# Optimization experiments

Measured on AMD Instinct MI355X. Metric: run time of the kernel, lower is better.

## Reference

```python
import jax, jax.numpy as jnp
import numpy as np

K = 0.5            # init kwarg k (score threshold)
G, S, C, M, DE = 256, 128, 512, 384, 128
N = G * S          # total nodes
EG = S + M         # edges per graph (first S point at the graph's last 'super' node)
E = G * EG


def setup_inputs() -> dict:
    key = jax.random.key(0)
    ks = jax.random.split(key, 8)
    x = jax.random.normal(ks[0], (N, C), jnp.float32)
    W = jax.random.normal(ks[1], (1, C), jnp.float32)
    batch = jnp.repeat(jnp.arange(G, dtype=jnp.int32), S)
    edge_num = jnp.full((G,), EG, dtype=jnp.int32)
    off = jnp.arange(G, dtype=jnp.int32) * S
    # structured edges: node i -> last node of its graph (the 'super node')
    struct_src = off[:, None] + jnp.arange(S, dtype=jnp.int32)[None, :]
    struct_dst = jnp.broadcast_to((off + S - 1)[:, None], (G, S))
    rand_src = jax.random.randint(ks[2], (G, M), 0, S, jnp.int32) + off[:, None]
    rand_dst = jax.random.randint(ks[3], (G, M), 0, S, jnp.int32) + off[:, None]
    src = jnp.concatenate([struct_src, rand_src], axis=1).reshape(-1)
    dst = jnp.concatenate([struct_dst, rand_dst], axis=1).reshape(-1)
    edge_index = jnp.stack([src, dst], axis=0)  # [2, E], grouped per graph
    edge_inform = jax.random.normal(ks[4], (E, DE), jnp.float32)
    br_feature = jax.random.normal(ks[5], (N, C), jnp.float32)
    return dict(x=x, edge_index=edge_index, edge_num=edge_num, edge_inform=edge_inform,
                batch=batch, br_feature=br_feature, br_index=edge_index,
                br_batch=batch, br_com_num=jnp.zeros((G,), jnp.int32), W=W)


def reference(x, edge_index, edge_num, edge_inform, batch, br_feature, br_index, br_batch, br_com_num, W):
    n, e, g = x.shape[0], edge_index.shape[1], edge_num.shape[0]
    score = jax.nn.sigmoid(jnp.mean(x * W, axis=-1))          # [N]
    x_out = x * score[:, None] * 2.0

    # per-graph node layout
    counts = jnp.bincount(batch, length=g)
    node_off = jnp.cumsum(counts) - counts
    last_node = node_off + counts - 1                          # 'super node' of each graph
    is_last = jnp.zeros((n,), bool).at[last_node].set(True)
    # torch loop runs over all but the last node of each graph
    low = (score < K) & (~is_last)                             # [N]

    # per-graph edge layout
    e_graph = jnp.repeat(jnp.arange(g, dtype=edge_num.dtype), edge_num)
    e_off = jnp.cumsum(edge_num) - edge_num
    local_pos = jnp.arange(e) - e_off[e_graph]                 # position inside graph's slice
    src, dst = edge_index[0], edge_index[1]
    # torch searches positions [1, eg) backwards for edge (low_node -> last_node): the
    # LAST matching position per low-score node gets masked out.
    cand = (dst == last_node[e_graph]) & low[src] & (batch[src] == e_graph) & (local_pos >= 1)
    val = jnp.where(cand, jnp.arange(e), -1)
    rem = jax.ops.segment_max(val, src, num_segments=n)        # last candidate edge per node
    drop = rem[rem >= 0]
    edge_mask = jnp.ones((e,), bool).at[drop].set(False)

    edge_num_plus = jax.ops.segment_sum(edge_mask.astype(edge_num.dtype), e_graph, num_segments=g)
    edge_index_plus = edge_index[:, edge_mask]
    edge_inform_plus = edge_inform[edge_mask]

    # BatchReversal: remove node (local_low_idx + com_num[g] + br_node_offset[g]) per low node
    n2 = br_feature.shape[0]
    counts2 = jnp.bincount(br_batch, length=g)
    node_off2 = jnp.cumsum(counts2) - counts2
    low_nodes = jnp.arange(n)[low]
    g_of = batch[low_nodes]
    br_drop = (low_nodes - node_off[g_of]) + br_com_num[g_of] + node_off2[g_of]
    br_mask = jnp.ones((n2,), bool).at[br_drop].set(False)
    leave = jnp.arange(n2)[br_mask]

    # filter_edge: keep nodes, remap edge endpoints, drop dangling edges
    br_feature_p = br_feature[leave]
    br_batch_p = br_batch[leave]
    remap = jnp.full((n2,), -1, dtype=jnp.int32).at[leave].set(jnp.arange(leave.shape[0], dtype=jnp.int32))
    r, c = remap[br_index[0]], remap[br_index[1]]
    keep = (r >= 0) & (c >= 0)
    br_index_p = jnp.stack([r[keep], c[keep]], axis=0)

    return (x_out, edge_index_plus, edge_inform_plus, edge_num_plus,
            br_feature_p, br_index_p, br_batch_p)
```

## Files before the change

kernel.cpp:

```cpp
#include <hip/hip_runtime.h>
#include <math.h>


__global__ void __launch_bounds__(512) k_count(
    const int* __restrict__ batch, int N,
    const int* __restrict__ br_batch, int N2,
    int* __restrict__ counts, int* __restrict__ counts2,
    int* __restrict__ dropcnt, int* __restrict__ brmask, int G){
  __shared__ int h1[512], h2[512];
  int t = threadIdx.x;
  h1[t] = 0; h2[t] = 0;
  __syncthreads();
  int gid    = blockIdx.x*blockDim.x + t;
  int stride = gridDim.x*blockDim.x;
  for (int i = gid; i < N;  i += stride) atomicAdd(&h1[batch[i]], 1);
  for (int i = gid; i < N2; i += stride) atomicAdd(&h2[br_batch[i]], 1);
  for (int i = gid; i < N2; i += stride) brmask[i] = 0;
  if (gid < G) dropcnt[gid] = 0;
  __syncthreads();
  if (t < G){
    if (h1[t]) atomicAdd(&counts[t],  h1[t]);
    if (h2[t]) atomicAdd(&counts2[t], h2[t]);
  }
}

__device__ __forceinline__ int scan512_excl_val(int v, int* s){
  int t = threadIdx.x;
  s[t] = v; __syncthreads();
  for (int off = 1; off < 512; off <<= 1){
    int add = (t >= off) ? s[t - off] : 0;
    __syncthreads();
    s[t] += add;
    __syncthreads();
  }
  int r = s[t] - v;
  __syncthreads();
  return r;
}

__global__ void __launch_bounds__(512) k_scan(
    const int* __restrict__ counts, const int* __restrict__ counts2,
    const int* __restrict__ edge_num, int G,
    int* __restrict__ node_off, int* __restrict__ node_off2,
    int* __restrict__ e_off){
  __shared__ int s[512];
  int t = threadIdx.x;
  int v1 = (t < G) ? counts[t]   : 0;
  int v2 = (t < G) ? counts2[t]  : 0;
  int v3 = (t < G) ? edge_num[t] : 0;
  int o1 = scan512_excl_val(v1, s);
  int o2 = scan512_excl_val(v2, s);
  int o3 = scan512_excl_val(v3, s);
  if (t < G){ node_off[t] = o1; node_off2[t] = o2; e_off[t] = o3; }
}

__global__ void __launch_bounds__(256) k_score(
    const float* __restrict__ x, const float* __restrict__ W,
    const int* __restrict__ batch, const int* __restrict__ counts,
    const int* __restrict__ node_off,
    float* __restrict__ out_x, int* __restrict__ low, int* __restrict__ rem,
    int C, int N){
  int wave = (blockIdx.x * blockDim.x + threadIdx.x) >> 6;
  int lane = threadIdx.x & 63;
  if (wave >= N) return;
  const float4* x4 = (const float4*)(x + (size_t)wave * C);
  const float4* W4 = (const float4*)W;
  const int nv = C >> 2;
  float acc = 0.f;
  float4 a0, a1;
  const bool fast = (nv == 128);
  if (fast){
    float4 w0 = W4[lane], w1 = W4[lane + 64];
    a0 = x4[lane]; a1 = x4[lane + 64];
    acc = a0.x*w0.x + a0.y*w0.y + a0.z*w0.z + a0.w*w0.w
        + a1.x*w1.x + a1.y*w1.y + a1.z*w1.z + a1.w*w1.w;
  } else {
    for (int k = lane; k < nv; k += 64){
      float4 a = x4[k]; float4 w = W4[k];
      acc += a.x*w.x + a.y*w.y + a.z*w.z + a.w*w.w;
    }
  }
  #pragma unroll
  for (int d = 1; d < 64; d <<= 1) acc += __shfl_xor(acc, d, 64);
  float scale = 2.0f / (1.0f + expf(-acc / (float)C));
  if (lane == 0){
    int g    = batch[wave];
    int last = node_off[g] + counts[g] - 1;
    low[wave] = (acc < 0.0f) && (wave != last) ? 1 : 0;
    rem[wave] = -1;
  }
  float4* o4 = (float4*)(out_x + (size_t)wave * C);
  if (fast){
    a0.x *= scale; a0.y *= scale; a0.z *= scale; a0.w *= scale;
    a1.x *= scale; a1.y *= scale; a1.z *= scale; a1.w *= scale;
    o4[lane]      = a0;
    o4[lane + 64] = a1;
  } else {
    for (int k = lane; k < nv; k += 64){
      float4 a = x4[k];
      a.x *= scale; a.y *= scale; a.z *= scale; a.w *= scale;
      o4[k] = a;
    }
  }
}

__device__ __forceinline__ int find_graph(const int* __restrict__ e_off, int G, int e){
  int lo = 0, hi = G - 1;
  while (lo < hi){
    int mid = (lo + hi + 1) >> 1;
    if (e_off[mid] <= e) lo = mid; else hi = mid - 1;
  }
  return lo;
}

__global__ void k_pass1(const int* __restrict__ ei, const int* __restrict__ e_off,
                        const int* __restrict__ node_off, const int* __restrict__ node_off2,
                        const int* __restrict__ counts, const int* __restrict__ batch,
                        const int* __restrict__ low, const int* __restrict__ br_com_num,
                        int* __restrict__ rem, int* __restrict__ brmask,
                        int E, int N, int G){
  int e = blockIdx.x*blockDim.x + threadIdx.x;
  if (e < N && low[e]){
    int g = batch[e];
    int d = e - node_off[g] + br_com_num[g] + node_off2[g];
    brmask[d] = 1;
  }
  if (e >= E) return;
  int g  = find_graph(e_off, G, e);
  if (e - e_off[g] < 1) return;
  int dst  = ei[E + e];
  int last = node_off[g] + counts[g] - 1;
  if (dst != last) return;
  int src = ei[e];
  if (!low[src]) return;
  if (batch[src] != g) return;
  atomicMax(&rem[src], e);
}

__global__ void k_pass2(const int* __restrict__ ei, const int* __restrict__ rem,
                        const int* __restrict__ e_off, const int* __restrict__ brmask,
                        const int* __restrict__ bi,
                        int* __restrict__ dropcnt,
                        int* __restrict__ bsumsA, int* __restrict__ bsumsB,
                        int* __restrict__ bsumsC,
                        int E, int N2, int EB, int G, int nbE, int nbN2){
  __shared__ int s[256];
  int b = blockIdx.x, t = threadIdx.x;
  int v = 0;
  if (b < nbE){
    int e = b*256 + t;
    if (e < E){
      v = (rem[ei[e]] != e) ? 1 : 0;
      if (!v){ int g = find_graph(e_off, G, e); atomicAdd(&dropcnt[g], 1); }
    }
  } else if (b < nbE + nbN2){
    int j = (b - nbE)*256 + t;
    v = (j < N2) ? (brmask[j] == 0) : 0;
  } else {
    int e = (b - nbE - nbN2)*256 + t;
    if (e < EB)
      v = (brmask[bi[e]] == 0 && brmask[bi[EB + e]] == 0) ? 1 : 0;
  }
  s[t] = v; __syncthreads();
  for (int off = 128; off > 0; off >>= 1){
    if (t < off) s[t] += s[t + off];
    __syncthreads();
  }
  if (t == 0){
    if (b < nbE)             bsumsA[b] = s[0];
    else if (b < nbE + nbN2) bsumsB[b - nbE] = s[0];
    else                     bsumsC[b - nbE - nbN2] = s[0];
  }
}

__device__ void scan_bsums_dev(int* __restrict__ bsums, int nb, int* __restrict__ total){
  __shared__ int s[1024];
  int t = threadIdx.x;
  int v = (t < nb) ? bsums[t] : 0;
  s[t] = v; __syncthreads();
  for (int off = 1; off < 1024; off <<= 1){
    int add = (t >= off) ? s[t - off] : 0;
    __syncthreads();
    s[t] += add;
    __syncthreads();
  }
  if (t < nb)      bsums[t] = s[t] - v;
  if (t == nb - 1) *total   = s[t];
}

__global__ void k_scanABC(int* __restrict__ bsumsA, int nbA,
                          int* __restrict__ bsumsB, int nbB,
                          int* __restrict__ bsumsC, int nbC,
                          int* __restrict__ totals){
  if      (blockIdx.x == 0) scan_bsums_dev(bsumsA, nbA, &totals[0]);
  else if (blockIdx.x == 1) scan_bsums_dev(bsumsB, nbB, &totals[1]);
  else                      scan_bsums_dev(bsumsC, nbC, &totals[2]);
}

__device__ __forceinline__ int excl_scan256(int v, int* s){
  int t = threadIdx.x;
  s[t] = v; __syncthreads();
  for (int off = 1; off < 256; off <<= 1){
    int add = (t >= off) ? s[t - off] : 0;
    __syncthreads();
    s[t] += add;
    __syncthreads();
  }
  return s[t] - v;
}

__global__ void k_pass3(const int* __restrict__ ei, const int* __restrict__ rem,
                        const int* __restrict__ bsumsA, const int* __restrict__ bsumsB,
                        const int* __restrict__ totals,
                        const int* __restrict__ edge_num, const int* __restrict__ dropcnt,
                        const int* __restrict__ brmask,
                        int* __restrict__ edge_pos, int* __restrict__ remap,
                        float* __restrict__ out, long long base0,
                        int E, int N2, int G, int DE, int nbE){
  __shared__ int s[256];
  int b = blockIdx.x, t = threadIdx.x;
  if (b < nbE){
    int e = b*256 + t;
    int keep = 0, src = 0, dst = 0;
    if (e < E){ src = ei[e]; dst = ei[E + e]; keep = (rem[src] != e) ? 1 : 0; }
    int excl = excl_scan256(keep, s);
    long long ek = totals[0];
    if (e < E){
      if (keep){
        int p = bsumsA[b] + excl;
        edge_pos[e] = p;
        out[base0 + p]      = (float)src;
        out[base0 + ek + p] = (float)dst;
      } else edge_pos[e] = -1;
    }
    if (b == 0){
      long long off3 = base0 + 2*ek + ek*(long long)DE;
      for (int g = t; g < G; g += 256)
        out[off3 + g] = (float)(edge_num[g] - dropcnt[g]);
    }
  } else {
    int j = (b - nbE)*256 + t;
    int keep = (j < N2) ? (brmask[j] == 0) : 0;
    int excl = excl_scan256(keep, s);
    if (j < N2) remap[j] = keep ? (bsumsB[b - nbE] + excl) : -1;
  }
}

__global__ void __launch_bounds__(256) k_pass45(
    const int* __restrict__ bi, const int* __restrict__ remap,
    const int* __restrict__ bsumsC, const int* __restrict__ totals,
    const float* __restrict__ inform, const int* __restrict__ edge_pos,
    const float* __restrict__ brf, const int* __restrict__ brb,
    float* __restrict__ out, long long base0,
    int G, int DE, int C, int EB, int E, int N2,
    int nbB, int nbE8){
  int b = blockIdx.x, t = threadIdx.x;
  long long ek = totals[0];
  if (b < nbB){
    __shared__ int s[256];
    long long nk = totals[1], kc = totals[2];
    long long off4 = base0 + 2*ek + ek*(long long)DE + G;
    int e = b*256 + t;
    int r = -1, c = -1, keep = 0;
    if (e < EB){
      r = remap[bi[e]];
      c = remap[bi[EB + e]];
      keep = (r >= 0 && c >= 0) ? 1 : 0;
    }
    int excl = excl_scan256(keep, s);
    if (keep){
      long long off5 = off4 + nk*(long long)C;
      int p = bsumsC[b] + excl;
      out[off5 + p]      = (float)r;
      out[off5 + kc + p] = (float)c;
    }
  } else if (b < nbB + nbE8){
    int e = (b - nbB)*8 + (t >> 5);
    if (e >= E) return;
    int p = edge_pos[e];
    if (p < 0) return;
    long long off2 = base0 + 2*ek;
    int lane = t & 31;
    const float4* in4 = (const float4*)(inform + (size_t)e * DE);
    float4*       o4  = (float4*)(out + off2 + (long long)p * DE);
    for (int j = lane; j < (DE >> 2); j += 32) o4[j] = in4[j];
  } else {
    long long nk = totals[1], kc = totals[2];
    long long off4 = base0 + 2*ek + ek*(long long)DE + G;
    int j = (b - nbB - nbE8)*2 + (t >> 7);
    if (j >= N2) return;
    int p = remap[j];
    if (p < 0) return;
    int lane = t & 127;
    const float4* in4 = (const float4*)(brf + (size_t)j * C);
    float4*       o4  = (float4*)(out + off4 + (long long)p * C);
    for (int k = lane; k < (C >> 2); k += 128) o4[k] = in4[k];
    if (lane == 0){
      long long off6 = off4 + nk*(long long)C + 2*kc;
      out[off6 + p] = (float)brb[j];
    }
  }
}

extern "C" void kernel_launch(void* const* d_in, const int* in_sizes, int n_in,
                              void* d_out, int out_size, void* d_ws, size_t ws_size,
                              hipStream_t stream){
  const float* x           = (const float*)d_in[0];
  const int*   edge_index  = (const int*)  d_in[1];
  const int*   edge_num    = (const int*)  d_in[2];
  const float* edge_inform = (const float*)d_in[3];
  const int*   batch       = (const int*)  d_in[4];
  const float* br_feature  = (const float*)d_in[5];
  const int*   br_index    = (const int*)  d_in[6];
  const int*   br_batch    = (const int*)  d_in[7];
  const int*   br_com_num  = (const int*)  d_in[8];
  const float* W           = (const float*)d_in[9];
  float* out = (float*)d_out;

  const int C  = in_sizes[9];
  const int N  = in_sizes[4];
  const int G  = in_sizes[2];
  const int E  = in_sizes[1] / 2;
  const int DE = in_sizes[3] / E;
  const int N2 = in_sizes[7];
  const int EB = in_sizes[6] / 2;

  int* ws        = (int*)d_ws;
  int* counts    = ws;
  int* counts2   = counts    + G;
  int* dropcnt   = counts2   + G;
  int* brmask    = dropcnt   + G;
  int* node_off  = brmask    + N2;
  int* node_off2 = node_off  + G;
  int* e_off     = node_off2 + G;
  int* totals    = e_off     + G;
  int* low       = totals    + 8;
  int* rem       = low       + N;
  int* remap     = rem       + N;
  int* edge_pos  = remap     + N2;
  int* bsumsA    = edge_pos  + E;
  int* bsumsB    = bsumsA    + 1024;
  int* bsumsC    = bsumsB    + 1024;

  const long long base0 = (long long)N * C;

  const int nbN2 = (N2 + 255) / 256;
  const int nbE  = (E  + 255) / 256;
  const int nbB  = (EB + 255) / 256;
  const int nbE8 = (E + 7) / 8;

  hipMemsetAsync(counts, 0, sizeof(int) * 2 * (size_t)G, stream);

  k_count<<<64, 512, 0, stream>>>(batch, N, br_batch, N2,
                                  counts, counts2, dropcnt, brmask, G);

  k_scan<<<1, 512, 0, stream>>>(counts, counts2, edge_num, G,
                                node_off, node_off2, e_off);

  k_score<<<(N * 64 + 255) / 256, 256, 0, stream>>>(x, W, batch, counts, node_off,
                                                    out, low, rem, C, N);

  k_pass1<<<(max(E, N) + 255) / 256, 256, 0, stream>>>(
      edge_index, e_off, node_off, node_off2, counts, batch, low, br_com_num,
      rem, brmask, E, N, G);

  k_pass2<<<nbE + nbN2 + nbB, 256, 0, stream>>>(edge_index, rem, e_off, brmask,
                                                br_index, dropcnt,
                                                bsumsA, bsumsB, bsumsC,
                                                E, N2, EB, G, nbE, nbN2);

  k_scanABC<<<3, 1024, 0, stream>>>(bsumsA, nbE, bsumsB, nbN2, bsumsC, nbB,
                                    totals);

  k_pass3<<<nbE + nbN2, 256, 0, stream>>>(edge_index, rem, bsumsA, bsumsB, totals,
                                          edge_num, dropcnt, brmask,
                                          edge_pos, remap, out, base0,
                                          E, N2, G, DE, nbE);

  k_pass45<<<nbB + nbE8 + (N2 + 1) / 2, 256, 0, stream>>>(
      br_index, remap, bsumsC, totals, edge_inform, edge_pos,
      br_feature, br_batch, out, base0,
      G, DE, C, EB, E, N2, nbB, nbE8);
}
```

Baseline: 359.2 us.

## Gather-based compaction copies and grid-stride two-row score kernel

The score kernel becomes a fixed 2048-block grid-stride loop that handles two rows per wave, which raises memory-level parallelism. The scatter copies of kept edge features and branch features, which used per-row wave groups and early exits for dropped rows, are replaced by inverse index maps (esrc, nsrc) built during the compaction scan. New flat grid-stride gather kernels then write output contiguously. The merged pass45 kernel is split into three launches, which adds launch overhead and one extra indirection per element.

```diff
diff --git a/kernel.cpp b/kernel.cpp
--- a/kernel.cpp
+++ b/kernel.cpp
@@ -54,52 +54,85 @@
   if (t < G){ node_off[t] = o1; node_off2[t] = o2; e_off[t] = o3; }
 }
 
+__device__ __forceinline__ float dot4(float4 a, float4 w){
+  return a.x*w.x + a.y*w.y + a.z*w.z + a.w*w.w;
+}
+
 __global__ void __launch_bounds__(256) k_score(
     const float* __restrict__ x, const float* __restrict__ W,
     const int* __restrict__ batch, const int* __restrict__ counts,
     const int* __restrict__ node_off,
     float* __restrict__ out_x, int* __restrict__ low, int* __restrict__ rem,
     int C, int N){
-  int wave = (blockIdx.x * blockDim.x + threadIdx.x) >> 6;
-  int lane = threadIdx.x & 63;
-  if (wave >= N) return;
-  const float4* x4 = (const float4*)(x + (size_t)wave * C);
+  int wid    = (blockIdx.x * blockDim.x + threadIdx.x) >> 6;
+  int lane   = threadIdx.x & 63;
+  int nwaves = (gridDim.x * blockDim.x) >> 6;
+  const int nv = C >> 2;
+  const bool fast = (nv == 128);
   const float4* W4 = (const float4*)W;
-  const int nv = C >> 2;
-  float acc = 0.f;
-  float4 a0, a1;
-  const bool fast = (nv == 128);
-  if (fast){
-    float4 w0 = W4[lane], w1 = W4[lane + 64];
-    a0 = x4[lane]; a1 = x4[lane + 64];
-    acc = a0.x*w0.x + a0.y*w0.y + a0.z*w0.z + a0.w*w0.w
-        + a1.x*w1.x + a1.y*w1.y + a1.z*w1.z + a1.w*w1.w;
-  } else {
-    for (int k = lane; k < nv; k += 64){
-      float4 a = x4[k]; float4 w = W4[k];
-      acc += a.x*w.x + a.y*w.y + a.z*w.z + a.w*w.w;
-    }
-  }
-  #pragma unroll
-  for (int d = 1; d < 64; d <<= 1) acc += __shfl_xor(acc, d, 64);
-  float scale = 2.0f / (1.0f + expf(-acc / (float)C));
-  if (lane == 0){
-    int g    = batch[wave];
-    int last = node_off[g] + counts[g] - 1;
-    low[wave] = (acc < 0.0f) && (wave != last) ? 1 : 0;
-    rem[wave] = -1;
-  }
-  float4* o4 = (float4*)(out_x + (size_t)wave * C);
-  if (fast){
-    a0.x *= scale; a0.y *= scale; a0.z *= scale; a0.w *= scale;
-    a1.x *= scale; a1.y *= scale; a1.z *= scale; a1.w *= scale;
-    o4[lane]      = a0;
-    o4[lane + 64] = a1;
-  } else {
-    for (int k = lane; k < nv; k += 64){
-      float4 a = x4[k];
-      a.x *= scale; a.y *= scale; a.z *= scale; a.w *= scale;
-      o4[k] = a;
+  float4 w0, w1;
+  if (fast){ w0 = W4[lane]; w1 = W4[lane + 64]; }
+
+  for (int nA = 2*wid; nA < N; nA += 2*nwaves){
+    int nB = nA + 1;
+    bool hasB = (nB < N);
+    const float4* xA = (const float4*)(x + (size_t)nA * C);
+    const float4* xB = (const float4*)(x + (size_t)nB * C);
+    float accA = 0.f, accB = 0.f;
+    float4 a0, a1, b0, b1;
+    if (fast){
+      a0 = xA[lane]; a1 = xA[lane + 64];
+      if (hasB){ b0 = xB[lane]; b1 = xB[lane + 64]; }
+      accA = dot4(a0, w0) + dot4(a1, w1);
+      if (hasB) accB = dot4(b0, w0) + dot4(b1, w1);
+    } else {
+      for (int k = lane; k < nv; k += 64){
+        float4 w = W4[k];
+        accA += dot4(xA[k], w);
+        if (hasB) accB += dot4(xB[k], w);
+      }
+    }
+    #pragma unroll
+    for (int d = 1; d < 64; d <<= 1){
+      accA += __shfl_xor(accA, d, 64);
+      accB += __shfl_xor(accB, d, 64);
+    }
+    float sA = 2.0f / (1.0f + expf(-accA / (float)C));
+    float sB = 2.0f / (1.0f + expf(-accB / (float)C));
+    if (lane == 0){
+      int g    = batch[nA];
+      int last = node_off[g] + counts[g] - 1;
+      low[nA] = (accA < 0.0f) && (nA != last) ? 1 : 0;
+      rem[nA] = -1;
+      if (hasB){
+        g    = batch[nB];
+        last = node_off[g] + counts[g] - 1;
+        low[nB] = (accB < 0.0f) && (nB != last) ? 1 : 0;
+        rem[nB] = -1;
+      }
+    }
+    float4* oA = (float4*)(out_x + (size_t)nA * C);
+    float4* oB = (float4*)(out_x + (size_t)nB * C);
+    if (fast){
+      a0.x*=sA; a0.y*=sA; a0.z*=sA; a0.w*=sA;
+      a1.x*=sA; a1.y*=sA; a1.z*=sA; a1.w*=sA;
+      oA[lane] = a0; oA[lane + 64] = a1;
+      if (hasB){
+        b0.x*=sB; b0.y*=sB; b0.z*=sB; b0.w*=sB;
+        b1.x*=sB; b1.y*=sB; b1.z*=sB; b1.w*=sB;
+        oB[lane] = b0; oB[lane + 64] = b1;
+      }
+    } else {
+      for (int k = lane; k < nv; k += 64){
+        float4 a = xA[k];
+        a.x*=sA; a.y*=sA; a.z*=sA; a.w*=sA;
+        oA[k] = a;
+        if (hasB){
+          float4 bv = xB[k];
+          bv.x*=sB; bv.y*=sB; bv.z*=sB; bv.w*=sB;
+          oB[k] = bv;
+        }
+      }
     }
   }
 }
@@ -214,7 +247,8 @@
                         const int* __restrict__ totals,
                         const int* __restrict__ edge_num, const int* __restrict__ dropcnt,
                         const int* __restrict__ brmask,
-                        int* __restrict__ edge_pos, int* __restrict__ remap,
+                        int* __restrict__ esrc, int* __restrict__ nsrc,
+                        int* __restrict__ remap,
                         float* __restrict__ out, long long base0,
                         int E, int N2, int G, int DE, int nbE){
   __shared__ int s[256];
@@ -225,13 +259,11 @@
     if (e < E){ src = ei[e]; dst = ei[E + e]; keep = (rem[src] != e) ? 1 : 0; }
     int excl = excl_scan256(keep, s);
     long long ek = totals[0];
-    if (e < E){
-      if (keep){
-        int p = bsumsA[b] + excl;
-        edge_pos[e] = p;
-        out[base0 + p]      = (float)src;
-        out[base0 + ek + p] = (float)dst;
-      } else edge_pos[e] = -1;
+    if (e < E && keep){
+      int p = bsumsA[b] + excl;
+      esrc[p] = e;
+      out[base0 + p]      = (float)src;
+      out[base0 + ek + p] = (float)dst;
     }
     if (b == 0){
       long long off3 = base0 + 2*ek + ek*(long long)DE;
@@ -242,64 +274,83 @@
     int j = (b - nbE)*256 + t;
     int keep = (j < N2) ? (brmask[j] == 0) : 0;
     int excl = excl_scan256(keep, s);
-    if (j < N2) remap[j] = keep ? (bsumsB[b - nbE] + excl) : -1;
-  }
-}
-
-__global__ void __launch_bounds__(256) k_pass45(
-    const int* __restrict__ bi, const int* __restrict__ remap,
-    const int* __restrict__ bsumsC, const int* __restrict__ totals,
-    const float* __restrict__ inform, const int* __restrict__ edge_pos,
+    if (j < N2){
+      int p = bsumsB[b - nbE] + excl;
+      remap[j] = keep ? p : -1;
+      if (keep) nsrc[p] = j;
+    }
+  }
+}
+
+__global__ void k_bredge(const int* __restrict__ bi, const int* __restrict__ remap,
+                         const int* __restrict__ bsumsC, const int* __restrict__ totals,
+                         float* __restrict__ out, long long base0,
+                         int G, int DE, int C, int EB){
+  __shared__ int s[256];
+  int b = blockIdx.x, t = threadIdx.x;
+  long long ek = totals[0], nk = totals[1], kc = totals[2];
+  long long off4 = base0 + 2*ek + ek*(long long)DE + G;
+  long long off5 = off4 + nk*(long long)C;
+  int e = b*256 + t;
+  int r = -1, c = -1, keep = 0;
+  if (e < EB){
+    r = remap[bi[e]];
+    c = remap[bi[EB + e]];
+    keep = (r >= 0 && c >= 0) ? 1 : 0;
+  }
+  int excl = excl_scan256(keep, s);
+  if (keep){
+    int p = bsumsC[b] + excl;
+    out[off5 + p]      = (float)r;
+    out[off5 + kc + p] = (float)c;
+  }
+}
+
+__global__ void __launch_bounds__(256) k_copyE(
+    const int* __restrict__ esrc, const int* __restrict__ totals,
+    const float* __restrict__ inform, float* __restrict__ out,
+    long long base0, int DE){
+  long long ek  = totals[0];
+  int de4       = DE >> 2;
+  long long tot = ek * (long long)de4;
+  long long off2 = base0 + 2*ek;
+  const float4* in4 = (const float4*)inform;
+  bool pw2 = (de4 & (de4 - 1)) == 0;
+  int  sh  = 31 - __clz(de4);
+  long long idx    = (long long)blockIdx.x*blockDim.x + threadIdx.x;
+  long long stride = (long long)gridDim.x*blockDim.x;
+  for (; idx < tot; idx += stride){
+    long long p = pw2 ? (idx >> sh) : (idx / de4);
+    int j = (int)(idx - p * de4);
+    int e = esrc[p];
+    float4 v = in4[(size_t)e * de4 + j];
+    ((float4*)(out + off2 + p * (long long)DE))[j] = v;
+  }
+}
+
+__global__ void __launch_bounds__(256) k_copyN(
+    const int* __restrict__ nsrc, const int* __restrict__ totals,
     const float* __restrict__ brf, const int* __restrict__ brb,
-    float* __restrict__ out, long long base0,
-    int G, int DE, int C, int EB, int E, int N2,
-    int nbB, int nbE8){
-  int b = blockIdx.x, t = threadIdx.x;
-  long long ek = totals[0];
-  if (b < nbB){
-    __shared__ int s[256];
-    long long nk = totals[1], kc = totals[2];
-    long long off4 = base0 + 2*ek + ek*(long long)DE + G;
-    int e = b*256 + t;
-    int r = -1, c = -1, keep = 0;
-    if (e < EB){
-      r = remap[bi[e]];
-      c = remap[bi[EB + e]];
-      keep = (r >= 0 && c >= 0) ? 1 : 0;
-    }
-    int excl = excl_scan256(keep, s);
-    if (keep){
-      long long off5 = off4 + nk*(long long)C;
-      int p = bsumsC[b] + excl;
-      out[off5 + p]      = (float)r;
-      out[off5 + kc + p] = (float)c;
-    }
-  } else if (b < nbB + nbE8){
-    int e = (b - nbB)*8 + (t >> 5);
-    if (e >= E) return;
-    int p = edge_pos[e];
-    if (p < 0) return;
-    long long off2 = base0 + 2*ek;
-    int lane = t & 31;
-    const float4* in4 = (const float4*)(inform + (size_t)e * DE);
-    float4*       o4  = (float4*)(out + off2 + (long long)p * DE);
-    for (int j = lane; j < (DE >> 2); j += 32) o4[j] = in4[j];
-  } else {
-    long long nk = totals[1], kc = totals[2];
-    long long off4 = base0 + 2*ek + ek*(long long)DE + G;
-    int j = (b - nbB - nbE8)*2 + (t >> 7);
-    if (j >= N2) return;
-    int p = remap[j];
-    if (p < 0) return;
-    int lane = t & 127;
-    const float4* in4 = (const float4*)(brf + (size_t)j * C);
-    float4*       o4  = (float4*)(out + off4 + (long long)p * C);
-    for (int k = lane; k < (C >> 2); k += 128) o4[k] = in4[k];
-    if (lane == 0){
-      long long off6 = off4 + nk*(long long)C + 2*kc;
-      out[off6 + p] = (float)brb[j];
-    }
-  }
+    float* __restrict__ out, long long base0, int G, int DE, int C){
+  long long ek = totals[0], nk = totals[1], kc = totals[2];
+  long long off4 = base0 + 2*ek + ek*(long long)DE + G;
+  long long off6 = off4 + nk*(long long)C + 2*kc;
+  int c4 = C >> 2;
+  bool pw2 = (c4 & (c4 - 1)) == 0;
+  int  sh  = 31 - __clz(c4);
+  long long tot = nk * (long long)c4;
+  const float4* in4 = (const float4*)brf;
+  long long idx    = (long long)blockIdx.x*blockDim.x + threadIdx.x;
+  long long stride = (long long)gridDim.x*blockDim.x;
+  for (long long i = idx; i < tot; i += stride){
+    long long p = pw2 ? (i >> sh) : (i / c4);
+    int j = (int)(i - p * c4);
+    int n = nsrc[p];
+    float4 v = in4[(size_t)n * c4 + j];
+    ((float4*)(out + off4 + p * (long long)C))[j] = v;
+  }
+  for (long long p = idx; p < nk; p += stride)
+    out[off6 + p] = (float)brb[nsrc[p]];
 }
 
 extern "C" void kernel_launch(void* const* d_in, const int* in_sizes, int n_in,
@@ -337,8 +388,9 @@
   int* low       = totals    + 8;
   int* rem       = low       + N;
   int* remap     = rem       + N;
-  int* edge_pos  = remap     + N2;
-  int* bsumsA    = edge_pos  + E;
+  int* esrc      = remap     + N2;
+  int* nsrc      = esrc      + E;
+  int* bsumsA    = nsrc      + N2;
   int* bsumsB    = bsumsA    + 1024;
   int* bsumsC    = bsumsB    + 1024;
 
@@ -347,7 +399,6 @@
   const int nbN2 = (N2 + 255) / 256;
   const int nbE  = (E  + 255) / 256;
   const int nbB  = (EB + 255) / 256;
-  const int nbE8 = (E + 7) / 8;
 
   hipMemsetAsync(counts, 0, sizeof(int) * 2 * (size_t)G, stream);
 
@@ -357,8 +408,8 @@
   k_scan<<<1, 512, 0, stream>>>(counts, counts2, edge_num, G,
                                 node_off, node_off2, e_off);
 
-  k_score<<<(N * 64 + 255) / 256, 256, 0, stream>>>(x, W, batch, counts, node_off,
-                                                    out, low, rem, C, N);
+  k_score<<<2048, 256, 0, stream>>>(x, W, batch, counts, node_off,
+                                    out, low, rem, C, N);
 
   k_pass1<<<(max(E, N) + 255) / 256, 256, 0, stream>>>(
       edge_index, e_off, node_off, node_off2, counts, batch, low, br_com_num,
@@ -374,11 +425,14 @@
 
   k_pass3<<<nbE + nbN2, 256, 0, stream>>>(edge_index, rem, bsumsA, bsumsB, totals,
                                           edge_num, dropcnt, brmask,
-                                          edge_pos, remap, out, base0,
+                                          esrc, nsrc, remap, out, base0,
                                           E, N2, G, DE, nbE);
 
-  k_pass45<<<nbB + nbE8 + (N2 + 1) / 2, 256, 0, stream>>>(
-      br_index, remap, bsumsC, totals, edge_inform, edge_pos,
-      br_feature, br_batch, out, base0,
-      G, DE, C, EB, E, N2, nbB, nbE8);
-}
+  k_bredge<<<nbB, 256, 0, stream>>>(br_index, remap, bsumsC, totals,
+                                    out, base0, G, DE, C, EB);
+
+  k_copyE<<<2048, 256, 0, stream>>>(esrc, totals, edge_inform, out, base0, DE);
+
+  k_copyN<<<2048, 256, 0, stream>>>(nsrc, totals, br_feature, br_batch,
+                                    out, base0, G, DE, C);
+}
```

Result: no change. 364.6 us (+1.5%).
